# Optimization experiments

Measured on AMD Instinct MI355X. Metric: run time of the kernel, lower is better.

Reference implementation:

```python
import jax, jax.numpy as jnp
import numpy as np

LEAK = 0.2
EPS_LN = 1e-5   # nn.LayerNorm default
EPS_IN = 1e-5   # nn.InstanceNorm2d default
EPS_D = 1e-8    # demodulation eps


def _leaky(x):
    return jnp.where(x >= 0, x, LEAK * x)


def _layernorm(s, g, b):
    mu = s.mean(-1, keepdims=True)
    v = ((s - mu) ** 2).mean(-1, keepdims=True)
    return (s - mu) / jnp.sqrt(v + EPS_LN) * g + b


def _instnorm(x):
    # per (b, c) normalization over HW, no affine (InstanceNorm2d default)
    mu = x.mean((2, 3), keepdims=True)
    v = ((x - mu) ** 2).mean((2, 3), keepdims=True)
    return (x - mu) / jnp.sqrt(v + EPS_IN)


def _conv(x, wt, pad):
    # x: [B,C,H,W], wt: [O,I,k,k]
    return jax.lax.conv_general_dilated(
        x, wt, (1, 1), [(pad, pad), (pad, pad)],
        dimension_numbers=('NCHW', 'OIHW', 'NCHW'))


def _modconv(x, w, wt, scale, mw, mb, lg, lb, asw, asb, abw, abb, demod):
    # style -> per-sample per-in-channel modulation
    s = _leaky(_layernorm(w @ mw.T + mb, lg, lb))              # [b, in]
    wb = wt[None] * (s[:, None, :, None, None] * scale[None])  # [b, O, I, k, k]
    # AdaIN on the input (use_adain=True in this block)
    sc = (w @ asw.T + asb)[:, :, None, None]
    bi = (w @ abw.T + abb)[:, :, None, None]
    x = sc * _instnorm(x) + bi
    if demod:
        d = jax.lax.rsqrt(jnp.sum(wb * wb, axis=(2, 3, 4)) + EPS_D)  # [b, O]
        wb = wb * d[:, :, None, None, None]
    pad = wt.shape[-1] // 2
    # per-sample conv == groups=b grouped conv in the torch original
    return jax.vmap(lambda xi, wi: _conv(xi[None], wi, pad)[0])(x, wb)


def _upsample2x(x):
    B, C, H, W = x.shape
    # bilinear, half-pixel centers == torch align_corners=False
    return jax.image.resize(x, (B, C, 2 * H, 2 * W), 'bilinear')


def setup_inputs() -> dict:
    key = jax.random.key(0)
    ks = iter(jax.random.split(key, 64))
    B, Cin, Cout, L, H = 8, 128, 64, 512, 128
    rn = lambda shape, s=1.0: jax.random.normal(next(ks), shape, jnp.float32) * s
    lin = 1.0 / float(np.sqrt(L))
    return dict(
        x=rn((B, Cin, H, H)), w=rn((B, L)),
        w1=rn((Cout, Cin, 3, 3), 0.02), sc1=jnp.ones((1, Cin, 1, 1), jnp.float32),
        m1_w=rn((Cin, L), lin), m1_b=jnp.zeros((Cin,), jnp.float32),
        ln1_g=jnp.ones((Cin,), jnp.float32), ln1_b=jnp.zeros((Cin,), jnp.float32),
        a1_sw=rn((Cin, L), lin), a1_sb=jnp.zeros((Cin,), jnp.float32),
        a1_bw=rn((Cin, L), lin), a1_bb=jnp.zeros((Cin,), jnp.float32),
        w25=rn((4, Cout, Cout, 3, 3), 0.02), sc25=jnp.ones((4, 1, Cout, 1, 1), jnp.float32),
        m25_w=rn((4, Cout, L), lin), m25_b=jnp.zeros((4, Cout), jnp.float32),
        ln25_g=jnp.ones((4, Cout), jnp.float32), ln25_b=jnp.zeros((4, Cout), jnp.float32),
        a25_sw=rn((4, Cout, L), lin), a25_sb=jnp.zeros((4, Cout), jnp.float32),
        a25_bw=rn((4, Cout, L), lin), a25_bb=jnp.zeros((4, Cout), jnp.float32),
        wr=rn((3, Cout, 1, 1), 0.02), scr=jnp.ones((1, Cout, 1, 1), jnp.float32),
        mr_w=rn((Cout, L), lin), mr_b=jnp.zeros((Cout,), jnp.float32),
        lnr_g=jnp.ones((Cout,), jnp.float32), lnr_b=jnp.zeros((Cout,), jnp.float32),
        ar_sw=rn((Cout, L), lin), ar_sb=jnp.zeros((Cout,), jnp.float32),
        ar_bw=rn((Cout, L), lin), ar_bb=jnp.zeros((Cout,), jnp.float32),
        sk_w=rn((Cout, Cin, 1, 1), 0.02), sk_b=jnp.zeros((Cout,), jnp.float32),
    )


def reference(x, w, w1, sc1, m1_w, m1_b, ln1_g, ln1_b, a1_sw, a1_sb, a1_bw, a1_bb,
              w25, sc25, m25_w, m25_b, ln25_g, ln25_b, a25_sw, a25_sb, a25_bw, a25_bb,
              wr, scr, mr_w, mr_b, lnr_g, lnr_b, ar_sw, ar_sb, ar_bw, ar_bb,
              sk_w, sk_b):
    x = _upsample2x(x)
    skip = _conv(x, sk_w, 0) + sk_b[None, :, None, None]
    h = _leaky(_modconv(x, w, w1, sc1, m1_w, m1_b, ln1_g, ln1_b,
                        a1_sw, a1_sb, a1_bw, a1_bb, True))
    for i in range(4):  # conv2..conv5, identical structure
        h = _leaky(_modconv(h, w, w25[i], sc25[i], m25_w[i], m25_b[i],
                            ln25_g[i], ln25_b[i], a25_sw[i], a25_sb[i],
                            a25_bw[i], a25_bb[i], True))
    h = h + skip
    rgb = _modconv(h, w, wr, scr, mr_w, mr_b, lnr_g, lnr_b,
                   ar_sw, ar_sb, ar_bw, ar_bb, False)
    return h, rgb
```

## Files before the change

### kernel.cpp

```cpp
#include <hip/hip_runtime.h>
#include <cstdint>

#define LEAK 0.2f

typedef __attribute__((ext_vector_type(8))) short bf16x8;
typedef __attribute__((ext_vector_type(4))) float f32x4;

__device__ __forceinline__ float leaky(float v){ return v >= 0.f ? v : LEAK*v; }

__device__ __forceinline__ uint32_t f32_to_bf16_rne(float v){
    uint32_t u = __float_as_uint(v);
    return (u + 0x7fffu + ((u >> 16) & 1u)) >> 16;
}
__device__ __forceinline__ uint32_t split_pack(float v){
    uint32_t u = __float_as_uint(v);
    uint32_t hb = (u + 0x7fffu + ((u >> 16) & 1u)) & 0xffff0000u;
    float lof = v - __uint_as_float(hb);
    uint32_t lo = f32_to_bf16_rne(lof);
    return (hb >> 16) | (lo << 16);
}

__global__ __launch_bounds__(128)
void style_kernel(const float* __restrict__ w,
                  const float* __restrict__ mw, const float* __restrict__ mb,
                  const float* __restrict__ lng, const float* __restrict__ lnb,
                  const float* __restrict__ asw, const float* __restrict__ asb,
                  const float* __restrict__ abw, const float* __restrict__ abb,
                  const float* __restrict__ sc, int Cin,
                  float* __restrict__ out_sm, float* __restrict__ out_asc,
                  float* __restrict__ out_abi)
{
    __shared__ float wl[512];
    __shared__ float red[128];
    int b = blockIdx.x;
    int tid = threadIdx.x;
    for (int j = tid; j < 512; j += 128) wl[j] = w[b*512 + j];
    __syncthreads();

    float t = 0.f, ascv = 0.f, abiv = 0.f;
    if (tid < Cin) {
        const float* r1 = mw  + (size_t)tid*512;
        const float* r2 = asw + (size_t)tid*512;
        const float* r3 = abw + (size_t)tid*512;
        for (int j = 0; j < 512; ++j) {
            float wj = wl[j];
            t    = fmaf(wj, r1[j], t);
            ascv = fmaf(wj, r2[j], ascv);
            abiv = fmaf(wj, r3[j], abiv);
        }
        t += mb[tid]; ascv += asb[tid]; abiv += abb[tid];
    }
    red[tid] = (tid < Cin) ? t : 0.f;
    __syncthreads();
    for (int s = 64; s > 0; s >>= 1) { if (tid < s) red[tid] += red[tid+s]; __syncthreads(); }
    float mu = red[0] / (float)Cin;
    __syncthreads();
    float dv = (tid < Cin) ? (t - mu) : 0.f;
    red[tid] = dv*dv;
    __syncthreads();
    for (int s = 64; s > 0; s >>= 1) { if (tid < s) red[tid] += red[tid+s]; __syncthreads(); }
    float var = red[0] / (float)Cin;
    float rstd = rsqrtf(var + 1e-5f);
    if (tid < Cin) {
        float sln = (t - mu) * rstd * lng[tid] + lnb[tid];
        sln = leaky(sln);
        out_sm[b*128 + tid]  = sln * sc[tid];
        out_asc[b*128 + tid] = ascv;
        out_abi[b*128 + tid] = abiv;
    }
}

__global__ __launch_bounds__(128)
void demod_kernel(const float* __restrict__ w1, const float* __restrict__ w25,
                  const float* __restrict__ sty, float* __restrict__ dout)
{
    int bid = blockIdx.x;
    int o = bid & 63;
    int b = (bid >> 6) & 7;
    int l = bid >> 9;
    int Cin = (l == 0) ? 128 : 64;
    const float* wt = (l == 0) ? (w1 + (size_t)o*128*9)
                               : (w25 + ((size_t)(l-1)*64 + o)*64*9);
    const float* smL = sty + l*3072 + b*128;
    int tid = threadIdx.x;
    float sum = 0.f;
    for (int i = tid; i < Cin; i += 128) {
        float s = smL[i];
        const float* wp = wt + i*9;
        float acc = 0.f;
        #pragma unroll
        for (int k = 0; k < 9; ++k) { float ww = wp[k]; acc = fmaf(ww, ww, acc); }
        sum = fmaf(acc, s*s, sum);
    }
    __shared__ float red[128];
    red[tid] = sum; __syncthreads();
    for (int s = 64; s > 0; s >>= 1) { if (tid < s) red[tid] += red[tid+s]; __syncthreads(); }
    if (tid == 0) dout[l*512 + b*64 + o] = rsqrtf(red[0] + 1e-8f);
}

__global__ __launch_bounds__(256)
void upsample_pack_kernel(const float* __restrict__ x, uint32_t* __restrict__ Up,
                          float* __restrict__ sums)
{
    int bid = blockIdx.x;
    int b = bid >> 8, y = bid & 255;
    int tid = threadIdx.x;
    int c = tid & 15, pg = tid >> 4;
    int q = y >> 1; int rlo, rhi; float wlo, whi;
    if (y & 1) { rlo = q; rhi = (q+1 < 127) ? q+1 : 127; wlo = 0.75f; whi = 0.25f; }
    else       { rlo = (q-1 > 0) ? q-1 : 0; rhi = q;     wlo = 0.25f; whi = 0.75f; }
    __shared__ float xs[2][16][129];
    __shared__ float red2[2][4][16];
    for (int cg = 0; cg < 8; ++cg) {
        __syncthreads();
        for (int e = tid; e < 4096; e += 256) {
            int row = e >> 11, cc = (e >> 7) & 15, px = e & 127;
            xs[row][cc][px] = x[((size_t)(b*128 + cg*16 + cc) << 14) + (row ? rhi : rlo)*128 + px];
        }
        __syncthreads();
        float s = 0.f, sq = 0.f;
        uint32_t* base = Up + ((((size_t)(b*8 + cg)*256 + y)*256))*16 + c;
        #pragma unroll
        for (int k = 0; k < 16; ++k) {
            int px = pg*16 + k;
            int m = px >> 1;
            float v;
            if (px & 1) {
                int m2 = (m+1 < 127) ? m+1 : 127;
                float vc = wlo*xs[0][c][m]  + whi*xs[1][c][m];
                float vr = wlo*xs[0][c][m2] + whi*xs[1][c][m2];
                v = 0.75f*vc + 0.25f*vr;
            } else {
                int m0 = (m-1 > 0) ? m-1 : 0;
                float vl = wlo*xs[0][c][m0] + whi*xs[1][c][m0];
                float vc = wlo*xs[0][c][m]  + whi*xs[1][c][m];
                v = 0.25f*vl + 0.75f*vc;
            }
            s += v; sq += v*v;
            base[(size_t)px*16] = split_pack(v);
        }
        s  += __shfl_xor(s, 16);  s  += __shfl_xor(s, 32);
        sq += __shfl_xor(sq, 16); sq += __shfl_xor(sq, 32);
        int wid = tid >> 6;
        if ((tid & 63) < 16) { red2[0][wid][c] = s; red2[1][wid][c] = sq; }
        __syncthreads();
        if (tid < 16) {
            float S = red2[0][0][tid] + red2[0][1][tid] + red2[0][2][tid] + red2[0][3][tid];
            float Q = red2[1][0][tid] + red2[1][1][tid] + red2[1][2][tid] + red2[1][3][tid];
            atomicAdd(&sums[(b*128 + cg*16 + tid)*2],     S);
            atomicAdd(&sums[(b*128 + cg*16 + tid)*2 + 1], Q);
        }
    }
}

__global__ __launch_bounds__(256)
void packskip_kernel(const float* __restrict__ skw, uint16_t* __restrict__ skp)
{
    int e = blockIdx.x*256 + threadIdx.x;
    if (e >= 8192) return;
    int o = e >> 7, i = e & 127;
    uint32_t pk = split_pack(skw[e]);
    int ic = i >> 4, cl = i & 15, cg = cl >> 2, j2 = (cl & 3)*2;
    uint16_t* dst = skp + ic*2048 + cg*512 + o*8 + j2;
    dst[0] = (uint16_t)(pk & 0xffffu);
    dst[1] = (uint16_t)(pk >> 16);
}

template<int CIN>
__global__ __launch_bounds__(CIN)
void packw_kernel(const float* __restrict__ wt, const float* __restrict__ sty,
                  const float* __restrict__ sums,
                  uint16_t* __restrict__ wp, float* __restrict__ bias9)
{
    int b = blockIdx.x >> 6;
    int o = blockIdx.x & 63;
    int i = threadIdx.x;

    float sm = sty[b*128 + i];
    float av = sty[1024 + b*128 + i];
    float bv = sty[2048 + b*128 + i];
    float s0 = sums[(b*CIN + i)*2], s1 = sums[(b*CIN + i)*2 + 1];
    float m = s0 * (1.f/65536.f);
    float var = s1 * (1.f/65536.f) - m*m;
    float r = rsqrtf((var > 0.f ? var : 0.f) + 1e-5f);
    float A  = sm * av * r;
    float Bv = sm * (bv - av*m*r);

    const float* wrow = wt + ((size_t)o*CIN + i)*9;
    float c9[9];
    #pragma unroll
    for (int k = 0; k < 9; ++k) c9[k] = wrow[k];

    const int NCH = CIN/16;
    int ic = i >> 4, cl = i & 15, cg = cl >> 2, j2 = (cl & 3)*2;
    uint16_t* wpb = wp + ((size_t)b*NCH + ic)*18432;
    #pragma unroll
    for (int k = 0; k < 9; ++k) {
        float wv = c9[k] * A;
        uint32_t pk = split_pack(wv);
        uint16_t* dst = wpb + k*2048 + cg*512 + o*8 + j2;
        dst[0] = (uint16_t)(pk & 0xffffu);
        dst[1] = (uint16_t)(pk >> 16);
    }

    float colS[3][3];
    #pragma unroll
    for (int ky = 0; ky < 3; ++ky) {
        colS[ky][0] = c9[ky*3+1] + c9[ky*3+2];
        colS[ky][1] = c9[ky*3+0] + c9[ky*3+1] + c9[ky*3+2];
        colS[ky][2] = c9[ky*3+0] + c9[ky*3+1];
    }
    float part[9];
    #pragma unroll
    for (int rx = 0; rx < 3; ++rx) {
        part[0*3+rx] = colS[1][rx] + colS[2][rx];
        part[1*3+rx] = colS[0][rx] + colS[1][rx] + colS[2][rx];
        part[2*3+rx] = colS[0][rx] + colS[1][rx];
    }
    __shared__ float red[9][CIN];
    #pragma unroll
    for (int t = 0; t < 9; ++t) red[t][i] = part[t] * Bv;
    __syncthreads();
    for (int s = CIN/2; s > 0; s >>= 1) {
        if (i < s) {
            #pragma unroll
            for (int t = 0; t < 9; ++t) red[t][i] += red[t][i + s];
        }
        __syncthreads();
    }
    if (i < 9) bias9[((size_t)(b*64 + o))*9 + i] = red[i][0];
}

template<int CIN, int MODE, bool SKIP>
__global__ __launch_bounds__(512)
void conv_mfma_kernel(const uint32_t* __restrict__ inPair,
                      const uint16_t* __restrict__ Wp,
                      const float* __restrict__ bias9,
                      const float* __restrict__ dmod,
                      const uint16_t* __restrict__ skp,
                      const float* __restrict__ skb,
                      float* __restrict__ skipOut,
                      uint32_t* __restrict__ outPair,
                      float* __restrict__ outF32,
                      float* __restrict__ statsH)
{
    __shared__ __align__(16) unsigned char LDS[78464];
    const int tid = threadIdx.x;
    const int lane = tid & 63, wv = tid >> 6;
    const int rw = wv >> 2, oq = wv & 3;

    int bid = blockIdx.x;
    bid = (bid & 7) * 256 + (bid >> 3);
    const int xh = bid & 1, yb = (bid >> 1) & 127, b = bid >> 8;
    const int y0 = yb*2, x0 = xh*128;

    union U8 { uint32_t u[4]; bf16x8 v; };

    f32x4 acc[8];
    f32x4 accS[SKIP ? 8 : 1];
    #pragma unroll
    for (int q = 0; q < 8; ++q) acc[q] = (f32x4){0.f, 0.f, 0.f, 0.f};
    if constexpr (SKIP) {
        #pragma unroll
        for (int q = 0; q < 8; ++q) accS[q] = (f32x4){0.f, 0.f, 0.f, 0.f};
    }

    const int NCH = CIN/16;
    for (int ic = 0; ic < NCH; ++ic) {
        uint4 sfrag;
        if constexpr (SKIP)
            sfrag = *reinterpret_cast<const uint4*>(
                skp + ic*2048 + (lane >> 4)*512 + (oq*16 + (lane & 15))*8);
        {
            const uint16_t* wsrc = Wp + ((size_t)b*NCH + ic)*18432;
            for (int e = tid; e < 2304; e += 512) {
                uint4 v = *reinterpret_cast<const uint4*>(wsrc + e*8);
                *reinterpret_cast<uint4*>(LDS + 41600 + e*16) = v;
            }
        }
        for (int e = tid; e < 2080; e += 512) {
            int part = e & 3;
            int pr = e >> 2;
            int px = pr % 130, row = pr / 130;
            int yy = y0 - 1 + row, xx = x0 - 1 + px;
            uint4 v = {0u, 0u, 0u, 0u};
            if (yy >= 0 && yy < 256 && xx >= 0 && xx < 256)
                v = *reinterpret_cast<const uint4*>(
                    inPair + ((((size_t)b*NCH + ic)*256 + yy)*256 + xx)*16 + part*4);
            *reinterpret_cast<uint4*>(LDS + row*10400 + px*80 + part*16) = v;
        }
        __syncthreads();
        #pragma unroll
        for (int tap = 0; tap < 9; ++tap) {
            const int dy1 = tap/3, dxm = tap % 3;
            uint4 wv4 = *reinterpret_cast<const uint4*>(
                LDS + 41600 + tap*4096 + (lane >> 4)*1024 + (oq*16 + (lane & 15))*16);
            U8 wa, wb;
            #pragma unroll
            for (int q = 0; q < 4; ++q) {
                uint32_t ww = (&wv4.x)[q];
                wa.u[q] = __builtin_amdgcn_perm(ww, ww, 0x01000100u);
                wb.u[q] = __builtin_amdgcn_perm(ww, ww, 0x03020302u);
            }
            U8 sa, sb;
            if constexpr (SKIP) {
                if (tap == 4) {
                    #pragma unroll
                    for (int q = 0; q < 4; ++q) {
                        uint32_t ww = (&sfrag.x)[q];
                        sa.u[q] = __builtin_amdgcn_perm(ww, ww, 0x01000100u);
                        sb.u[q] = __builtin_amdgcn_perm(ww, ww, 0x03020302u);
                    }
                }
            }
            const int rowbase = (rw + dy1)*10400 + (lane >> 4)*16 + ((lane & 15) + dxm)*80;
            #pragma unroll
            for (int xf = 0; xf < 8; ++xf) {
                bf16x8 bf = *reinterpret_cast<const bf16x8*>(LDS + rowbase + xf*1280);
                acc[xf] = __builtin_amdgcn_mfma_f32_16x16x32_bf16(wa.v, bf, acc[xf], 0, 0, 0);
                acc[xf] = __builtin_amdgcn_mfma_f32_16x16x32_bf16(wb.v, bf, acc[xf], 0, 0, 0);
                if constexpr (SKIP) {
                    if (tap == 4) {
                        accS[xf] = __builtin_amdgcn_mfma_f32_16x16x32_bf16(sa.v, bf, accS[xf], 0, 0, 0);
                        accS[xf] = __builtin_amdgcn_mfma_f32_16x16x32_bf16(sb.v, bf, accS[xf], 0, 0, 0);
                    }
                }
            }
        }
        __syncthreads();
    }

    const int y = y0 + rw;
    const int ry = (y == 0) ? 0 : ((y == 255) ? 2 : 1);
    float dv4[4], bmid[4], bl[4], br[4], skb4[4];
    #pragma unroll
    for (int r2 = 0; r2 < 4; ++r2) {
        int o = oq*16 + (lane >> 4)*4 + r2;
        dv4[r2] = dmod[b*64 + o];
        const float* bp = bias9 + ((size_t)(b*64 + o))*9 + ry*3;
        bmid[r2] = bp[1];
        bl[r2] = bmid[r2]; br[r2] = bmid[r2];
        if (x0 == 0   && (lane & 15) == 0)  bl[r2] = bp[0];
        if (x0 == 128 && (lane & 15) == 15) br[r2] = bp[2];
        if constexpr (SKIP) skb4[r2] = skb[o];
    }

    float s4[4] = {0.f,0.f,0.f,0.f}, q4[4] = {0.f,0.f,0.f,0.f};
    #pragma unroll
    for (int xf = 0; xf < 8; ++xf) {
        #pragma unroll
        for (int r2 = 0; r2 < 4; ++r2) {
            float bias = (xf == 0) ? bl[r2] : ((xf == 7) ? br[r2] : bmid[r2]);
            float v = (acc[xf][r2] + bias) * dv4[r2];
            v = leaky(v);
            acc[xf][r2] = v;
            if (MODE != 2) { s4[r2] += v; q4[r2] += v*v; }
        }
    }

    if constexpr (SKIP) {
        #pragma unroll
        for (int xf = 0; xf < 8; ++xf) {
            #pragma unroll
            for (int r2 = 0; r2 < 4; ++r2) {
                int o = oq*16 + (lane >> 4)*4 + r2;
                size_t addr = ((size_t)(b*64 + o))*65536 + (size_t)y*256 + x0 + xf*16 + (lane & 15);
                skipOut[addr] = accS[xf][r2] + skb4[r2];
            }
        }
    }

    if constexpr (MODE == 2) {
        #pragma unroll
        for (int xf = 0; xf < 8; ++xf) {
            #pragma unroll
            for (int r2 = 0; r2 < 4; ++r2) {
                int o = oq*16 + (lane >> 4)*4 + r2;
                size_t addr = ((size_t)(b*64 + o))*65536 + (size_t)y*256 + x0 + xf*16 + (lane & 15);
                float v = acc[xf][r2] + outF32[addr];
                outF32[addr] = v;
                s4[r2] += v; q4[r2] += v*v;
            }
        }
    }

    #pragma unroll
    for (int r2 = 0; r2 < 4; ++r2) {
        #pragma unroll
        for (int w = 1; w < 16; w <<= 1) {
            s4[r2] += __shfl_xor(s4[r2], w);
            q4[r2] += __shfl_xor(q4[r2], w);
        }
    }
    if ((lane & 15) == 0) {
        #pragma unroll
        for (int r2 = 0; r2 < 4; ++r2) {
            int o = oq*16 + (lane >> 4)*4 + r2;
            atomicAdd(&statsH[(b*64 + o)*2],     s4[r2]);
            atomicAdd(&statsH[(b*64 + o)*2 + 1], q4[r2]);
        }
    }

    if constexpr (MODE != 2) {
        for (int ph = 0; ph < 2; ++ph) {
            __syncthreads();
            if (rw == ph) {
                #pragma unroll
                for (int xf = 0; xf < 8; ++xf) {
                    int px = xf*16 + (lane & 15);
                    uint4 pk4;
                    pk4.x = split_pack(acc[xf][0]);
                    pk4.y = split_pack(acc[xf][1]);
                    pk4.z = split_pack(acc[xf][2]);
                    pk4.w = split_pack(acc[xf][3]);
                    *reinterpret_cast<uint4*>(
                        LDS + ((px*256 + oq*64 + (lane >> 4)*16) ^ ((px & 15) << 4))) = pk4;
                }
            }
            __syncthreads();
            int px = tid >> 2, s = tid & 3;
            #pragma unroll
            for (int q = 0; q < 4; ++q) {
                uint4 v = *reinterpret_cast<const uint4*>(
                    LDS + ((px*256 + q*64 + s*16) ^ ((px & 15) << 4)));
                *reinterpret_cast<uint4*>(
                    outPair + ((((size_t)b*4 + q)*256 + (y0 + ph))*256 + x0 + px)*16 + s*4) = v;
            }
        }
    }
}

__global__ __launch_bounds__(256)
void rgb_kernel(const float* __restrict__ h, const float* __restrict__ wr,
                const float* __restrict__ sty, const float* __restrict__ sums,
                float* __restrict__ rgb)
{
    __shared__ float A[64], Bc[64];
    __shared__ float wl[192];
    int bid = blockIdx.x;
    int b = bid >> 7;
    int px0 = (bid & 127) * 512;
    int tid = threadIdx.x;
    if (tid < 64) {
        float smv = sty[b*128 + tid];
        float av  = sty[1024 + b*128 + tid];
        float bv  = sty[2048 + b*128 + tid];
        float s0 = sums[(b*64 + tid)*2], s1 = sums[(b*64 + tid)*2 + 1];
        float m = s0 * (1.f/65536.f);
        float var = s1 * (1.f/65536.f) - m*m;
        float r = rsqrtf((var > 0.f ? var : 0.f) + 1e-5f);
        A[tid]  = smv * av * r;
        Bc[tid] = smv * (bv - av*m*r);
    }
    if (tid < 192) wl[tid] = wr[tid];
    __syncthreads();
    int pix = px0 + tid*2;
    const float* hp = h + (size_t)b*64*65536 + pix;
    float a0[3] = {0,0,0}, a1[3] = {0,0,0};
    for (int i = 0; i < 64; ++i) {
        float2 v = *reinterpret_cast<const float2*>(hp + (size_t)i*65536);
        float xi0 = fmaf(A[i], v.x, Bc[i]);
        float xi1 = fmaf(A[i], v.y, Bc[i]);
        #pragma unroll
        for (int o = 0; o < 3; ++o) {
            float wv = wl[o*64 + i];
            a0[o] = fmaf(wv, xi0, a0[o]);
            a1[o] = fmaf(wv, xi1, a1[o]);
        }
    }
    float* rp = rgb + (size_t)b*3*65536 + pix;
    #pragma unroll
    for (int o = 0; o < 3; ++o)
        *reinterpret_cast<float2*>(rp + (size_t)o*65536) = make_float2(a0[o], a1[o]);
}

extern "C" void kernel_launch(void* const* d_in, const int* in_sizes, int n_in,
                              void* d_out, int out_size, void* d_ws, size_t ws_size,
                              hipStream_t stream)
{
    const float* x     = (const float*)d_in[0];
    const float* w     = (const float*)d_in[1];
    const float* w1    = (const float*)d_in[2];
    const float* sc1   = (const float*)d_in[3];
    const float* m1_w  = (const float*)d_in[4];
    const float* m1_b  = (const float*)d_in[5];
    const float* ln1_g = (const float*)d_in[6];
    const float* ln1_b = (const float*)d_in[7];
    const float* a1_sw = (const float*)d_in[8];
    const float* a1_sb = (const float*)d_in[9];
    const float* a1_bw = (const float*)d_in[10];
    const float* a1_bb = (const float*)d_in[11];
    const float* w25   = (const float*)d_in[12];
    const float* sc25  = (const float*)d_in[13];
    const float* m25_w = (const float*)d_in[14];
    const float* m25_b = (const float*)d_in[15];
    const float* ln25_g= (const float*)d_in[16];
    const float* ln25_b= (const float*)d_in[17];
    const float* a25_sw= (const float*)d_in[18];
    const float* a25_sb= (const float*)d_in[19];
    const float* a25_bw= (const float*)d_in[20];
    const float* a25_bb= (const float*)d_in[21];
    const float* wr    = (const float*)d_in[22];
    const float* scr   = (const float*)d_in[23];
    const float* mr_w  = (const float*)d_in[24];
    const float* mr_b  = (const float*)d_in[25];
    const float* lnr_g = (const float*)d_in[26];
    const float* lnr_b = (const float*)d_in[27];
    const float* ar_sw = (const float*)d_in[28];
    const float* ar_sb = (const float*)d_in[29];
    const float* ar_bw = (const float*)d_in[30];
    const float* ar_bb = (const float*)d_in[31];
    const float* sk_w  = (const float*)d_in[32];
    const float* sk_b  = (const float*)d_in[33];

    float* outp    = (float*)d_out;
    float* h_out   = outp;
    float* rgb_out = outp + (size_t)33554432;

    uint8_t* ws = (uint8_t*)d_ws;
    uint32_t*  Upair  = (uint32_t*)(ws + 0);
    uint32_t*  hpB    = (uint32_t*)(ws + 0);
    uint32_t*  hpA    = (uint32_t*)(ws + 268435456ull);
    uint16_t*  WpBase = (uint16_t*)(ws + 402653184ull);
    float*     sty    = (float*)(ws + 409731072ull);
    float*     dmod   = (float*)(ws + 409804800ull);
    float*     stats  = (float*)(ws + 409815040ull);
    float*     bias9  = (float*)(ws + 409843712ull);
    uint16_t*  skp    = (uint16_t*)(ws + 409935872ull);

    float* sumsU = stats;
    float* st1   = stats + 2048;
    float* st2   = stats + 3072;
    float* st3   = stats + 4096;
    float* st4   = stats + 5120;
    float* st5   = stats + 6144;

    uint16_t* Wp1 = WpBase;
    uint16_t* Wp2 = WpBase + 1179648;
    uint16_t* Wp3 = Wp2 + 589824;
    uint16_t* Wp4 = Wp3 + 589824;
    uint16_t* Wp5 = Wp4 + 589824;

    hipMemsetAsync(stats, 0, 28672, stream);

    style_kernel<<<8,128,0,stream>>>(w, m1_w, m1_b, ln1_g, ln1_b, a1_sw, a1_sb,
                                     a1_bw, a1_bb, sc1, 128,
                                     sty, sty+1024, sty+2048);
    for (int l = 1; l <= 4; ++l) {
        int j = l - 1;
        style_kernel<<<8,128,0,stream>>>(w, m25_w + (size_t)j*32768, m25_b + j*64,
                                         ln25_g + j*64, ln25_b + j*64,
                                         a25_sw + (size_t)j*32768, a25_sb + j*64,
                                         a25_bw + (size_t)j*32768, a25_bb + j*64,
                                         sc25 + j*64, 64,
                                         sty + l*3072, sty + l*3072 + 1024, sty + l*3072 + 2048);
    }
    style_kernel<<<8,128,0,stream>>>(w, mr_w, mr_b, lnr_g, lnr_b, ar_sw, ar_sb,
                                     ar_bw, ar_bb, scr, 64,
                                     sty + 5*3072, sty + 5*3072 + 1024, sty + 5*3072 + 2048);

    demod_kernel<<<2560,128,0,stream>>>(w1, w25, sty, dmod);
    packskip_kernel<<<32,256,0,stream>>>(sk_w, skp);

    upsample_pack_kernel<<<2048,256,0,stream>>>(x, Upair, sumsU);

    packw_kernel<128><<<512,128,0,stream>>>(w1, sty, sumsU, Wp1, bias9);
    conv_mfma_kernel<128,1,true><<<2048,512,0,stream>>>(Upair, Wp1, bias9, dmod,
                                                        skp, sk_b, h_out,
                                                        hpA, nullptr, st1);
    packw_kernel<64><<<512,64,0,stream>>>(w25, sty + 3072, st1, Wp2, bias9 + 4608);
    conv_mfma_kernel<64,1,false><<<2048,512,0,stream>>>(hpA, Wp2, bias9 + 4608, dmod + 512,
                                                        nullptr, nullptr, nullptr,
                                                        hpB, nullptr, st2);
    packw_kernel<64><<<512,64,0,stream>>>(w25 + 36864, sty + 2*3072, st2, Wp3, bias9 + 2*4608);
    conv_mfma_kernel<64,1,false><<<2048,512,0,stream>>>(hpB, Wp3, bias9 + 2*4608, dmod + 2*512,
                                                        nullptr, nullptr, nullptr,
                                                        hpA, nullptr, st3);
    packw_kernel<64><<<512,64,0,stream>>>(w25 + 2*36864, sty + 3*3072, st3, Wp4, bias9 + 3*4608);
    conv_mfma_kernel<64,1,false><<<2048,512,0,stream>>>(hpA, Wp4, bias9 + 3*4608, dmod + 3*512,
                                                        nullptr, nullptr, nullptr,
                                                        hpB, nullptr, st4);
    packw_kernel<64><<<512,64,0,stream>>>(w25 + 3*36864, sty + 4*3072, st4, Wp5, bias9 + 4*4608);
    conv_mfma_kernel<64,2,false><<<2048,512,0,stream>>>(hpB, Wp5, bias9 + 4*4608, dmod + 4*512,
                                                        nullptr, nullptr, nullptr,
                                                        nullptr, h_out, st5);

    rgb_kernel<<<1024,256,0,stream>>>(h_out, wr, sty + 5*3072, st5, rgb_out);
}
```

Baseline: 1.508 ms.

## Add remapped conv kernel with 2x2 output-channel/pixel wave tiling and block swizzle

Result: slower. 1.828 ms (+21.2%).

```diff
diff --git a/kernel.cpp b/kernel.cpp
--- a/kernel.cpp
+++ b/kernel.cpp
@@ -161,7 +161,7 @@
     int o = e >> 7, i = e & 127;
     uint32_t pk = split_pack(skw[e]);
     int ic = i >> 4, cl = i & 15, cg = cl >> 2, j2 = (cl & 3)*2;
-    uint16_t* dst = skp + ic*2048 + cg*512 + o*8 + j2;
+    uint16_t* dst = skp + ic*2048 + (o >> 4)*512 + cg*128 + (o & 15)*8 + j2;
     dst[0] = (uint16_t)(pk & 0xffffu);
     dst[1] = (uint16_t)(pk >> 16);
 }
@@ -198,7 +198,7 @@
     for (int k = 0; k < 9; ++k) {
         float wv = c9[k] * A;
         uint32_t pk = split_pack(wv);
-        uint16_t* dst = wpb + k*2048 + cg*512 + o*8 + j2;
+        uint16_t* dst = wpb + k*2048 + (o >> 4)*512 + cg*128 + (o & 15)*8 + j2;
         dst[0] = (uint16_t)(pk & 0xffffu);
         dst[1] = (uint16_t)(pk >> 16);
     }
@@ -270,7 +270,7 @@
         uint4 sfrag;
         if constexpr (SKIP)
             sfrag = *reinterpret_cast<const uint4*>(
-                skp + ic*2048 + (lane >> 4)*512 + (oq*16 + (lane & 15))*8);
+                skp + ic*2048 + oq*512 + (lane >> 4)*128 + (lane & 15)*8);
         {
             const uint16_t* wsrc = Wp + ((size_t)b*NCH + ic)*18432;
             for (int e = tid; e < 2304; e += 512) {
@@ -294,7 +294,7 @@
         for (int tap = 0; tap < 9; ++tap) {
             const int dy1 = tap/3, dxm = tap % 3;
             uint4 wv4 = *reinterpret_cast<const uint4*>(
-                LDS + 41600 + tap*4096 + (lane >> 4)*1024 + (oq*16 + (lane & 15))*16);
+                LDS + 41600 + tap*4096 + oq*1024 + (lane >> 4)*256 + (lane & 15)*16);
             U8 wa, wb;
             #pragma unroll
             for (int q = 0; q < 4; ++q) {
@@ -416,6 +416,189 @@
                     *reinterpret_cast<uint4*>(
                         LDS + ((px*256 + oq*64 + (lane >> 4)*16) ^ ((px & 15) << 4))) = pk4;
                 }
+            }
+            __syncthreads();
+            int px = tid >> 2, s = tid & 3;
+            #pragma unroll
+            for (int q = 0; q < 4; ++q) {
+                uint4 v = *reinterpret_cast<const uint4*>(
+                    LDS + ((px*256 + q*64 + s*16) ^ ((px & 15) << 4)));
+                *reinterpret_cast<uint4*>(
+                    outPair + ((((size_t)b*4 + q)*256 + (y0 + ph))*256 + x0 + px)*16 + s*4) = v;
+            }
+        }
+    }
+}
+
+template<int MODE>
+__global__ __launch_bounds__(512)
+void conv_mfma_remap_kernel(const uint32_t* __restrict__ inPair,
+                            const uint16_t* __restrict__ Wp,
+                            const float* __restrict__ bias9,
+                            const float* __restrict__ dmod,
+                            uint32_t* __restrict__ outPair,
+                            float* __restrict__ outF32,
+                            float* __restrict__ statsH)
+{
+    __shared__ __align__(16) unsigned char LDS[78464];
+    const int tid = threadIdx.x;
+    const int lane = tid & 63, wvi = tid >> 6;
+    const int rw = wvi >> 2, xh = (wvi >> 1) & 1, oh = wvi & 1;
+
+    int bid = blockIdx.x;
+    bid = (bid & 7) * 256 + (bid >> 3);
+    const int xhb = bid & 1, yb = (bid >> 1) & 127, b = bid >> 8;
+    const int y0 = yb*2, x0 = xhb*128;
+
+    union U8 { uint32_t u[4]; bf16x8 v; };
+
+    f32x4 acc[4][2];
+    #pragma unroll
+    for (int xfl = 0; xfl < 4; ++xfl) {
+        acc[xfl][0] = (f32x4){0.f, 0.f, 0.f, 0.f};
+        acc[xfl][1] = (f32x4){0.f, 0.f, 0.f, 0.f};
+    }
+
+    for (int ic = 0; ic < 4; ++ic) {
+        {
+            const uint16_t* wsrc = Wp + ((size_t)b*4 + ic)*18432;
+            for (int e = tid; e < 2304; e += 512) {
+                uint4 v = *reinterpret_cast<const uint4*>(wsrc + e*8);
+                *reinterpret_cast<uint4*>(LDS + 41600 + e*16) = v;
+            }
+        }
+        for (int e = tid; e < 2080; e += 512) {
+            int part = e & 3;
+            int pr = e >> 2;
+            int px = pr % 130, row = pr / 130;
+            int yy = y0 - 1 + row, xx = x0 - 1 + px;
+            uint4 v = {0u, 0u, 0u, 0u};
+            if (yy >= 0 && yy < 256 && xx >= 0 && xx < 256)
+                v = *reinterpret_cast<const uint4*>(
+                    inPair + ((((size_t)b*4 + ic)*256 + yy)*256 + xx)*16 + part*4);
+            *reinterpret_cast<uint4*>(LDS + row*10400 + px*80 + part*16) = v;
+        }
+        __syncthreads();
+        #pragma unroll
+        for (int tap = 0; tap < 9; ++tap) {
+            const int dy1 = tap/3, dxm = tap % 3;
+            U8 wa0, wb0, wa1, wb1;
+            {
+                uint4 w0 = *reinterpret_cast<const uint4*>(
+                    LDS + 41600 + tap*4096 + (oh*2+0)*1024 + (lane >> 4)*256 + (lane & 15)*16);
+                uint4 w1 = *reinterpret_cast<const uint4*>(
+                    LDS + 41600 + tap*4096 + (oh*2+1)*1024 + (lane >> 4)*256 + (lane & 15)*16);
+                #pragma unroll
+                for (int q = 0; q < 4; ++q) {
+                    uint32_t u0 = (&w0.x)[q], u1 = (&w1.x)[q];
+                    wa0.u[q] = __builtin_amdgcn_perm(u0, u0, 0x01000100u);
+                    wb0.u[q] = __builtin_amdgcn_perm(u0, u0, 0x03020302u);
+                    wa1.u[q] = __builtin_amdgcn_perm(u1, u1, 0x01000100u);
+                    wb1.u[q] = __builtin_amdgcn_perm(u1, u1, 0x03020302u);
+                }
+            }
+            const int rowbase = (rw + dy1)*10400 + (lane >> 4)*16
+                              + ((lane & 15) + xh*64 + dxm)*80;
+            #pragma unroll
+            for (int xfl = 0; xfl < 4; ++xfl) {
+                bf16x8 bf = *reinterpret_cast<const bf16x8*>(LDS + rowbase + xfl*1280);
+                acc[xfl][0] = __builtin_amdgcn_mfma_f32_16x16x32_bf16(wa0.v, bf, acc[xfl][0], 0, 0, 0);
+                acc[xfl][1] = __builtin_amdgcn_mfma_f32_16x16x32_bf16(wa1.v, bf, acc[xfl][1], 0, 0, 0);
+                acc[xfl][0] = __builtin_amdgcn_mfma_f32_16x16x32_bf16(wb0.v, bf, acc[xfl][0], 0, 0, 0);
+                acc[xfl][1] = __builtin_amdgcn_mfma_f32_16x16x32_bf16(wb1.v, bf, acc[xfl][1], 0, 0, 0);
+            }
+        }
+        __syncthreads();
+    }
+
+    const int y = y0 + rw;
+    const int ry = (y == 0) ? 0 : ((y == 255) ? 2 : 1);
+    float dv4[2][4], bmid[2][4], bl4[2][4], br4[2][4];
+    #pragma unroll
+    for (int ofl = 0; ofl < 2; ++ofl)
+        #pragma unroll
+        for (int r2 = 0; r2 < 4; ++r2) {
+            int o = (oh*2+ofl)*16 + (lane >> 4)*4 + r2;
+            dv4[ofl][r2] = dmod[b*64 + o];
+            const float* bp = bias9 + ((size_t)(b*64 + o))*9 + ry*3;
+            bmid[ofl][r2] = bp[1];
+            bl4[ofl][r2] = bmid[ofl][r2]; br4[ofl][r2] = bmid[ofl][r2];
+            if (x0 == 0   && xh == 0 && (lane & 15) == 0)  bl4[ofl][r2] = bp[0];
+            if (x0 == 128 && xh == 1 && (lane & 15) == 15) br4[ofl][r2] = bp[2];
+        }
+
+    float s4[2][4] = {{0.f,0.f,0.f,0.f},{0.f,0.f,0.f,0.f}};
+    float q4[2][4] = {{0.f,0.f,0.f,0.f},{0.f,0.f,0.f,0.f}};
+    #pragma unroll
+    for (int xfl = 0; xfl < 4; ++xfl) {
+        bool isL = (xh == 0 && xfl == 0), isR = (xh == 1 && xfl == 3);
+        #pragma unroll
+        for (int ofl = 0; ofl < 2; ++ofl)
+            #pragma unroll
+            for (int r2 = 0; r2 < 4; ++r2) {
+                float bias = isL ? bl4[ofl][r2] : (isR ? br4[ofl][r2] : bmid[ofl][r2]);
+                float v = (acc[xfl][ofl][r2] + bias) * dv4[ofl][r2];
+                v = leaky(v);
+                acc[xfl][ofl][r2] = v;
+                if (MODE != 2) { s4[ofl][r2] += v; q4[ofl][r2] += v*v; }
+            }
+    }
+
+    if constexpr (MODE == 2) {
+        #pragma unroll
+        for (int xfl = 0; xfl < 4; ++xfl)
+            #pragma unroll
+            for (int ofl = 0; ofl < 2; ++ofl)
+                #pragma unroll
+                for (int r2 = 0; r2 < 4; ++r2) {
+                    int o = (oh*2+ofl)*16 + (lane >> 4)*4 + r2;
+                    size_t addr = ((size_t)(b*64 + o))*65536 + (size_t)y*256
+                                + x0 + (xh*4+xfl)*16 + (lane & 15);
+                    float v = acc[xfl][ofl][r2] + outF32[addr];
+                    outF32[addr] = v;
+                    s4[ofl][r2] += v; q4[ofl][r2] += v*v;
+                }
+    }
+
+    #pragma unroll
+    for (int ofl = 0; ofl < 2; ++ofl)
+        #pragma unroll
+        for (int r2 = 0; r2 < 4; ++r2) {
+            #pragma unroll
+            for (int w = 1; w < 16; w <<= 1) {
+                s4[ofl][r2] += __shfl_xor(s4[ofl][r2], w);
+                q4[ofl][r2] += __shfl_xor(q4[ofl][r2], w);
+            }
+        }
+    if ((lane & 15) == 0) {
+        #pragma unroll
+        for (int ofl = 0; ofl < 2; ++ofl)
+            #pragma unroll
+            for (int r2 = 0; r2 < 4; ++r2) {
+                int o = (oh*2+ofl)*16 + (lane >> 4)*4 + r2;
+                atomicAdd(&statsH[(b*64 + o)*2],     s4[ofl][r2]);
+                atomicAdd(&statsH[(b*64 + o)*2 + 1], q4[ofl][r2]);
+            }
+    }
+
+    if constexpr (MODE != 2) {
+        for (int ph = 0; ph < 2; ++ph) {
+            __syncthreads();
+            if (rw == ph) {
+                #pragma unroll
+                for (int xfl = 0; xfl < 4; ++xfl)
+                    #pragma unroll
+                    for (int ofl = 0; ofl < 2; ++ofl) {
+                        int px = (xh*4+xfl)*16 + (lane & 15);
+                        int obase = oh*128 + ofl*64 + (lane >> 4)*16;
+                        uint4 pk4;
+                        pk4.x = split_pack(acc[xfl][ofl][0]);
+                        pk4.y = split_pack(acc[xfl][ofl][1]);
+                        pk4.z = split_pack(acc[xfl][ofl][2]);
+                        pk4.w = split_pack(acc[xfl][ofl][3]);
+                        *reinterpret_cast<uint4*>(
+                            LDS + ((px*256 + obase) ^ ((px & 15) << 4))) = pk4;
+                    }
             }
             __syncthreads();
             int px = tid >> 2, s = tid & 3;
@@ -569,21 +752,17 @@
                                                         skp, sk_b, h_out,
                                                         hpA, nullptr, st1);
     packw_kernel<64><<<512,64,0,stream>>>(w25, sty + 3072, st1, Wp2, bias9 + 4608);
-    conv_mfma_kernel<64,1,false><<<2048,512,0,stream>>>(hpA, Wp2, bias9 + 4608, dmod + 512,
-                                                        nullptr, nullptr, nullptr,
-                                                        hpB, nullptr, st2);
+    conv_mfma_remap_kernel<1><<<2048,512,0,stream>>>(hpA, Wp2, bias9 + 4608, dmod + 512,
+                                                     hpB, nullptr, st2);
     packw_kernel<64><<<512,64,0,stream>>>(w25 + 36864, sty + 2*3072, st2, Wp3, bias9 + 2*4608);
-    conv_mfma_kernel<64,1,false><<<2048,512,0,stream>>>(hpB, Wp3, bias9 + 2*4608, dmod + 2*512,
-                                                        nullptr, nullptr, nullptr,
-                                                        hpA, nullptr, st3);
+    conv_mfma_remap_kernel<1><<<2048,512,0,stream>>>(hpB, Wp3, bias9 + 2*4608, dmod + 2*512,
+                                                     hpA, nullptr, st3);
     packw_kernel<64><<<512,64,0,stream>>>(w25 + 2*36864, sty + 3*3072, st3, Wp4, bias9 + 3*4608);
-    conv_mfma_kernel<64,1,false><<<2048,512,0,stream>>>(hpA, Wp4, bias9 + 3*4608, dmod + 3*512,
-                                                        nullptr, nullptr, nullptr,
-                                                        hpB, nullptr, st4);
+    conv_mfma_remap_kernel<1><<<2048,512,0,stream>>>(hpA, Wp4, bias9 + 3*4608, dmod + 3*512,
+                                                     hpB, nullptr, st4);
     packw_kernel<64><<<512,64,0,stream>>>(w25 + 3*36864, sty + 4*3072, st4, Wp5, bias9 + 4*4608);
-    conv_mfma_kernel<64,2,false><<<2048,512,0,stream>>>(hpB, Wp5, bias9 + 4*4608, dmod + 4*512,
-                                                        nullptr, nullptr, nullptr,
-                                                        nullptr, h_out, st5);
+    conv_mfma_remap_kernel<2><<<2048,512,0,stream>>>(hpB, Wp5, bias9 + 4*4608, dmod + 4*512,
+                                                     nullptr, h_out, st5);
 
     rgb_kernel<<<1024,256,0,stream>>>(h_out, wr, sty + 5*3072, st5, rgb_out);
 }
```
